# Performance work log

Measured on AMD Instinct MI355X. Metric: run time of the kernel, lower is better.

## Reference

```python
import jax, jax.numpy as jnp
import numpy as np

B, C, IMG, PS, S, D, H, HD, L, OUT = 512, 3, 36, 6, 36, 768, 12, 64, 4, 256

def _pos_embedding(seq_len, dim):
    # NOTE: cos at even indices, sin at odd (as in the torch source)
    position = np.arange(seq_len, dtype=np.float32)[:, None]
    div = np.exp(np.arange(0, dim, 2, dtype=np.float32) * -(np.log(10000.0) / dim))
    emb = np.zeros((seq_len, dim), dtype=np.float32)
    emb[:, 0::2] = np.cos(position * div)
    emb[:, 1::2] = np.sin(position * div)
    return jnp.asarray(emb)

def setup_inputs():
    ks = jax.random.split(jax.random.key(0), 10)
    sc = lambda f: 1.0 / np.sqrt(f)
    return {
        'batch': jax.random.normal(ks[0], (B, C, IMG, IMG), jnp.float32),
        'W_patch': jax.random.normal(ks[1], (D, PS * PS), jnp.float32) * sc(PS * PS),
        'b_patch': jnp.zeros((D,), jnp.float32),
        'pos': _pos_embedding(S, D),
        'ln1_g': jnp.ones((L, D), jnp.float32),
        'ln1_b': jnp.zeros((L, D), jnp.float32),
        'Wq': jax.random.normal(ks[2], (L, H, HD, HD), jnp.float32) * sc(HD),
        'bq': jnp.zeros((L, H, HD), jnp.float32),
        'Wk': jax.random.normal(ks[3], (L, H, HD, HD), jnp.float32) * sc(HD),
        'bk': jnp.zeros((L, H, HD), jnp.float32),
        'Wv': jax.random.normal(ks[4], (L, H, HD, HD), jnp.float32) * sc(HD),
        'bv': jnp.zeros((L, H, HD), jnp.float32),
        'ln2_g': jnp.ones((L, D), jnp.float32),
        'ln2_b': jnp.zeros((L, D), jnp.float32),
        'W1': jax.random.normal(ks[5], (L, 2 * D, D), jnp.float32) * sc(D),
        'b1': jnp.zeros((L, 2 * D), jnp.float32),
        'W2': jax.random.normal(ks[6], (L, D, 2 * D), jnp.float32) * sc(2 * D),
        'b2': jnp.zeros((L, D), jnp.float32),
        'W_out': jax.random.normal(ks[7], (OUT, D), jnp.float32) * sc(D),
        'b_out': jnp.zeros((OUT,), jnp.float32),
    }

def _layernorm(x, g, b):
    m = jnp.mean(x, axis=-1, keepdims=True)
    v = jnp.mean((x - m) ** 2, axis=-1, keepdims=True)
    return (x - m) / jnp.sqrt(v + 1e-5) * g + b

def _forward(batch, W_patch, b_patch, pos, ln1_g, ln1_b, Wq, bq, Wk, bk, Wv, bv,
             ln2_g, ln2_b, W1, b1, W2, b2, W_out, b_out):
    b_, c_ = batch.shape[0], batch.shape[1]
    # patchify: (B,C,36,36) -> (B,C,36 patches,36 pixels), matching torch unfold+reshape
    p = batch.reshape(b_, c_, IMG // PS, PS, IMG // PS, PS)
    p = p.transpose(0, 1, 2, 4, 3, 5).reshape(b_, c_, S, PS * PS)
    z = p @ W_patch.T + b_patch + pos  # pos broadcasts over (B,C)
    scale = 1.0 / np.sqrt(HD)
    for l in range(L):
        # pre-LN then batched per-head attention (collapses the python loops)
        h = _layernorm(z, ln1_g[l], ln1_b[l]).reshape(b_, c_, S, H, HD)
        q = jnp.einsum('bcshd,hed->bcshe', h, Wq[l]) + bq[l]
        k = jnp.einsum('bcshd,hed->bcshe', h, Wk[l]) + bk[l]
        v = jnp.einsum('bcshd,hed->bcshe', h, Wv[l]) + bv[l]
        attn = jax.nn.softmax(jnp.einsum('bcshe,bcthe->bchst', q, k) * scale, axis=-1)
        o = jnp.einsum('bchst,bcthe->bcshe', attn, v).reshape(b_, c_, S, D)
        z = z + o
        z = _layernorm(z, ln2_g[l], ln2_b[l])
        z = z + (jax.nn.relu(z @ W1[l].T + b1[l]) @ W2[l].T + b2[l])
    return z @ W_out.T + b_out

def reference(batch, W_patch, b_patch, pos, ln1_g, ln1_b, Wq, bq, Wk, bk, Wv, bv,
              ln2_g, ln2_b, W1, b1, W2, b2, W_out, b_out):
    return _forward(batch, W_patch, b_patch, pos, ln1_g, ln1_b, Wq, bq, Wk, bk, Wv, bv,
                    ln2_g, ln2_b, W1, b1, W2, b2, W_out, b_out)
```

## Files before the change

### kernel.cpp

```cpp
#include <hip/hip_runtime.h>
#include <hip/hip_bf16.h>
#include <cstdint>
#include <cstddef>

typedef __bf16 bf16;
typedef bf16 bf16x8 __attribute__((ext_vector_type(8)));
typedef bf16 bf16x4 __attribute__((ext_vector_type(4)));
typedef float f32x4 __attribute__((ext_vector_type(4)));
typedef unsigned int u32;

#define GLD_LDS16(gptr, lptr)                                                        \
  __builtin_amdgcn_global_load_lds((const __attribute__((address_space(1))) u32*)(gptr), \
                                   (__attribute__((address_space(3))) u32*)(lptr), 16, 0, 0)

static constexpr int S = 36, D = 768, H = 12, HD = 64, DFF = 1536;
static constexpr int BC = 1536;
static constexpr int M = BC * S;
static constexpr int OUTD = 256;

__global__ __launch_bounds__(256) void f2b_kernel(const float* __restrict__ in,
                                                  bf16* __restrict__ out, int n4) {
  int i = blockIdx.x * 256 + threadIdx.x;
  if (i < n4) {
    float4 f = ((const float4*)in)[i];
    bf16x4 o = {(bf16)f.x, (bf16)f.y, (bf16)f.z, (bf16)f.w};
    ((bf16x4*)out)[i] = o;
  }
}

__global__ __launch_bounds__(256) void patch_embed(const float* __restrict__ batch,
                                                   const float* __restrict__ Wp,
                                                   const float* __restrict__ bp,
                                                   const float* __restrict__ pos,
                                                   float* __restrict__ z) {
  int bc = blockIdx.x, tid = threadIdx.x;
  __shared__ float p[36][40];
  for (int i = tid; i < 1296; i += 256) {
    float f = batch[(size_t)bc * 1296 + i];
    int row = i / 36, col = i - row * 36;
    p[(row / 6) * 6 + col / 6][(row % 6) * 6 + (col % 6)] = f;
  }
  __syncthreads();
  for (int c0 = 0; c0 < 768; c0 += 256) {
    int d = c0 + tid;
    float wr[36];
    const float4* wp4 = (const float4*)(Wp + (size_t)d * 36);
#pragma unroll
    for (int q = 0; q < 9; ++q) {
      float4 f = wp4[q];
      wr[q * 4] = f.x; wr[q * 4 + 1] = f.y; wr[q * 4 + 2] = f.z; wr[q * 4 + 3] = f.w;
    }
    float gb = bp[d];
    for (int s = 0; s < 36; ++s) {
      float acc = 0.f;
#pragma unroll
      for (int k = 0; k < 36; ++k) acc += p[s][k] * wr[k];
      z[((size_t)bc * 36 + s) * 768 + d] = acc + gb + pos[s * 768 + d];
    }
  }
}

__global__ __launch_bounds__(256) void ln_stats(const float* __restrict__ zin,
                                                float* __restrict__ stats) {
  int row = blockIdx.x * 4 + (threadIdx.x >> 6);
  int lane = threadIdx.x & 63;
  const float* zr = zin + (size_t)row * D;
  float x[12];
#pragma unroll
  for (int i = 0; i < 12; ++i) x[i] = zr[i * 64 + lane];
  float s = 0.f;
#pragma unroll
  for (int i = 0; i < 12; ++i) s += x[i];
#pragma unroll
  for (int off = 32; off >= 1; off >>= 1) s += __shfl_xor(s, off, 64);
  float m = s * (1.f / 768.f);
  float v = 0.f;
#pragma unroll
  for (int i = 0; i < 12; ++i) { float dd = x[i] - m; v += dd * dd; }
#pragma unroll
  for (int off = 32; off >= 1; off >>= 1) v += __shfl_xor(v, off, 64);
  v *= (1.f / 768.f);
  if (lane == 0) {
    stats[(size_t)row * 2] = m;
    stats[(size_t)row * 2 + 1] = rsqrtf(v + 1e-5f);
  }
}

__global__ __launch_bounds__(256) void ln_inplace(float* __restrict__ z,
                                                  const float* __restrict__ g,
                                                  const float* __restrict__ bt) {
  int row = blockIdx.x * 4 + (threadIdx.x >> 6);
  int lane = threadIdx.x & 63;
  float* zr = z + (size_t)row * D;
  float x[12];
#pragma unroll
  for (int i = 0; i < 12; ++i) x[i] = zr[i * 64 + lane];
  float s = 0.f;
#pragma unroll
  for (int i = 0; i < 12; ++i) s += x[i];
#pragma unroll
  for (int off = 32; off >= 1; off >>= 1) s += __shfl_xor(s, off, 64);
  float m = s * (1.f / 768.f);
  float v = 0.f;
#pragma unroll
  for (int i = 0; i < 12; ++i) { float dd = x[i] - m; v += dd * dd; }
#pragma unroll
  for (int off = 32; off >= 1; off >>= 1) v += __shfl_xor(v, off, 64);
  v *= (1.f / 768.f);
  float rstd = rsqrtf(v + 1e-5f);
#pragma unroll
  for (int i = 0; i < 12; ++i) {
    int d = i * 64 + lane;
    zr[d] = (x[i] - m) * rstd * g[d] + bt[d];
  }
}

__global__ __launch_bounds__(64) void attn_kernel(const float* __restrict__ zg,
                                                  const float* __restrict__ stats,
                                                  const float* __restrict__ g1,
                                                  const float* __restrict__ b1_,
                                                  const bf16* __restrict__ Wq,
                                                  const bf16* __restrict__ Wk,
                                                  const bf16* __restrict__ Wv,
                                                  const float* __restrict__ bq,
                                                  const float* __restrict__ bk,
                                                  const float* __restrict__ bv,
                                                  float* __restrict__ z) {
  int head = blockIdx.x;
  int bc = blockIdx.y;
  __shared__ __align__(16) bf16 qb[48 * 72];
  __shared__ __align__(16) bf16 kb[48 * 72];
  __shared__ __align__(16) bf16 vt[64 * 72];
  int lane = threadIdx.x;
  int lr = lane & 15, quad = lane >> 4;

#pragma unroll
  for (int t0 = 0; t0 < 16; ++t0) vt[lane * 72 + 48 + t0] = (bf16)0.f;

  const float* zsrc = zg + ((size_t)bc * S) * D + head * HD;
  const float* st = stats + (size_t)bc * S * 2;

  float gv[2][8], bvv[2][8];
#pragma unroll
  for (int kt = 0; kt < 2; ++kt) {
    int c0 = head * HD + kt * 32 + quad * 8;
    float4 ga = *(const float4*)(g1 + c0);
    float4 gb2 = *(const float4*)(g1 + c0 + 4);
    float4 ba = *(const float4*)(b1_ + c0);
    float4 bb2 = *(const float4*)(b1_ + c0 + 4);
    gv[kt][0] = ga.x; gv[kt][1] = ga.y; gv[kt][2] = ga.z; gv[kt][3] = ga.w;
    gv[kt][4] = gb2.x; gv[kt][5] = gb2.y; gv[kt][6] = gb2.z; gv[kt][7] = gb2.w;
    bvv[kt][0] = ba.x; bvv[kt][1] = ba.y; bvv[kt][2] = ba.z; bvv[kt][3] = ba.w;
    bvv[kt][4] = bb2.x; bvv[kt][5] = bb2.y; bvv[kt][6] = bb2.z; bvv[kt][7] = bb2.w;
  }

  bf16x8 hfrag[3][2];
#pragma unroll
  for (int mt = 0; mt < 3; ++mt) {
    int srow = mt * 16 + lr;
    if (srow < 36) {
      float mm = st[srow * 2], rr = st[srow * 2 + 1];
#pragma unroll
      for (int kt = 0; kt < 2; ++kt) {
        int c0 = kt * 32 + quad * 8;
        float4 f0 = *(const float4*)(zsrc + (size_t)srow * D + c0);
        float4 f1 = *(const float4*)(zsrc + (size_t)srow * D + c0 + 4);
        float hv[8] = {f0.x, f0.y, f0.z, f0.w, f1.x, f1.y, f1.z, f1.w};
        bf16x8 o;
#pragma unroll
        for (int j = 0; j < 8; ++j) o[j] = (bf16)((hv[j] - mm) * rr * gv[kt][j] + bvv[kt][j]);
        hfrag[mt][kt] = o;
      }
    } else {
#pragma unroll
      for (int kt = 0; kt < 2; ++kt) {
        bf16x8 o;
#pragma unroll
        for (int j = 0; j < 8; ++j) o[j] = (bf16)0.f;
        hfrag[mt][kt] = o;
      }
    }
  }

  const bf16* Wm[3] = {Wq + (size_t)head * 4096, Wk + (size_t)head * 4096, Wv + (size_t)head * 4096};
  const float* Bm[3] = {bq + head * 64, bk + head * 64, bv + head * 64};
  for (int p = 0; p < 3; ++p) {
    bf16x8 bfr[4][2];
#pragma unroll
    for (int nt = 0; nt < 4; ++nt)
#pragma unroll
      for (int kt = 0; kt < 2; ++kt)
        bfr[nt][kt] = *(const bf16x8*)(Wm[p] + (nt * 16 + lr) * 64 + kt * 32 + quad * 8);
#pragma unroll
    for (int mt = 0; mt < 3; ++mt) {
      f32x4 acc[4] = {};
#pragma unroll
      for (int kt = 0; kt < 2; ++kt)
#pragma unroll
        for (int nt = 0; nt < 4; ++nt)
          acc[nt] = __builtin_amdgcn_mfma_f32_16x16x32_bf16(hfrag[mt][kt], bfr[nt][kt], acc[nt], 0, 0, 0);
#pragma unroll
      for (int nt = 0; nt < 4; ++nt) {
        float bb = Bm[p][nt * 16 + lr];
#pragma unroll
        for (int r = 0; r < 4; ++r) {
          int s2 = mt * 16 + quad * 4 + r;
          int e = nt * 16 + lr;
          float val = acc[nt][r] + bb;
          if (p == 0) qb[s2 * 72 + e] = (bf16)val;
          else if (p == 1) kb[s2 * 72 + e] = (bf16)val;
          else vt[e * 72 + s2] = (bf16)val;
        }
      }
    }
  }
  __syncthreads();

  f32x4 sc[3][3];
#pragma unroll
  for (int mt = 0; mt < 3; ++mt)
#pragma unroll
    for (int nt = 0; nt < 3; ++nt) {
      f32x4 a = {};
#pragma unroll
      for (int kt = 0; kt < 2; ++kt) {
        bf16x8 af = *(const bf16x8*)&qb[(mt * 16 + lr) * 72 + kt * 32 + quad * 8];
        bf16x8 bf_ = *(const bf16x8*)&kb[(nt * 16 + lr) * 72 + kt * 32 + quad * 8];
        a = __builtin_amdgcn_mfma_f32_16x16x32_bf16(af, bf_, a, 0, 0, 0);
      }
      int t = nt * 16 + lr;
#pragma unroll
      for (int r = 0; r < 4; ++r) {
        float v = a[r] * 0.125f;
        if (t >= 36) v = -1e30f;
        sc[mt][nt][r] = v;
      }
    }
  __syncthreads();

#pragma unroll
  for (int mt = 0; mt < 3; ++mt) {
    float mx[4], sum[4];
#pragma unroll
    for (int r = 0; r < 4; ++r)
      mx[r] = fmaxf(fmaxf(sc[mt][0][r], sc[mt][1][r]), sc[mt][2][r]);
#pragma unroll
    for (int r = 0; r < 4; ++r)
#pragma unroll
      for (int off = 8; off >= 1; off >>= 1) mx[r] = fmaxf(mx[r], __shfl_xor(mx[r], off, 64));
#pragma unroll
    for (int r = 0; r < 4; ++r) sum[r] = 0.f;
#pragma unroll
    for (int nt = 0; nt < 3; ++nt)
#pragma unroll
      for (int r = 0; r < 4; ++r) {
        float e = __expf(sc[mt][nt][r] - mx[r]);
        sc[mt][nt][r] = e;
        sum[r] += e;
      }
#pragma unroll
    for (int r = 0; r < 4; ++r)
#pragma unroll
      for (int off = 8; off >= 1; off >>= 1) sum[r] += __shfl_xor(sum[r], off, 64);
#pragma unroll
    for (int nt = 0; nt < 4; ++nt)
#pragma unroll
      for (int r = 0; r < 4; ++r) {
        int s2 = mt * 16 + quad * 4 + r;
        int t = nt * 16 + lr;
        float pv = (nt < 3) ? sc[mt][nt][r] / sum[r] : 0.f;
        qb[s2 * 72 + t] = (bf16)pv;
      }
  }
  __syncthreads();

#pragma unroll
  for (int mt = 0; mt < 3; ++mt) {
    f32x4 o[4] = {};
#pragma unroll
    for (int kt = 0; kt < 2; ++kt) {
      bf16x8 a = *(const bf16x8*)&qb[(mt * 16 + lr) * 72 + kt * 32 + quad * 8];
#pragma unroll
      for (int nt = 0; nt < 4; ++nt) {
        bf16x8 b = *(const bf16x8*)&vt[(nt * 16 + lr) * 72 + kt * 32 + quad * 8];
        o[nt] = __builtin_amdgcn_mfma_f32_16x16x32_bf16(a, b, o[nt], 0, 0, 0);
      }
    }
#pragma unroll
    for (int nt = 0; nt < 4; ++nt)
#pragma unroll
      for (int r = 0; r < 4; ++r) {
        int s2 = mt * 16 + quad * 4 + r;
        if (s2 < 36) {
          int e = nt * 16 + lr;
          size_t idx = ((size_t)bc * S + s2) * D + head * HD + e;
          z[idx] += o[nt][r];
        }
      }
  }
}

template <int N, int K, int MODE, int AF32>
__global__ __launch_bounds__(256) void gemm_bt(const void* __restrict__ A,
                                               const bf16* __restrict__ Bw,
                                               const float* __restrict__ bias,
                                               const float* __restrict__ res,
                                               void* __restrict__ outp) {
  constexpr int BK = 64;
  __shared__ __align__(16) bf16 As[128 * BK];
  __shared__ __align__(16) bf16 Bs[128 * BK];
  int tid = threadIdx.x;
  int bn = blockIdx.x, bm = blockIdx.y;
  const bf16* Abf = (const bf16*)A + (size_t)bm * 128 * K;
  const float* Af = (const float*)A + (size_t)bm * 128 * K;
  const bf16* Bb = Bw + (size_t)bn * 128 * K;
  int lane = tid & 63, wave = tid >> 6;
  int wm = (wave >> 1) * 64, wn = (wave & 1) * 64;
  int lr = lane & 15, quad = lane >> 4;
  f32x4 acc[4][4] = {};
  for (int k0 = 0; k0 < K; k0 += BK) {
    if (AF32) {
#pragma unroll
      for (int r = 0; r < 8; ++r) {
        int c = r * 256 + tid;
        int row = c >> 4, col4 = (c & 15) * 4;
        float4 f = *(const float4*)(Af + (size_t)row * K + k0 + col4);
        bf16x4 o = {(bf16)f.x, (bf16)f.y, (bf16)f.z, (bf16)f.w};
        *(bf16x4*)&As[row * BK + col4] = o;
      }
    } else {
#pragma unroll
      for (int r = 0; r < 4; ++r) {
        int c = r * 256 + tid;
        int row = c >> 3, col = (c & 7) * 8;
        GLD_LDS16(Abf + (size_t)row * K + k0 + col, &As[c * 8]);
      }
    }
#pragma unroll
    for (int r = 0; r < 4; ++r) {
      int c = r * 256 + tid;
      int row = c >> 3, col = (c & 7) * 8;
      GLD_LDS16(Bb + (size_t)row * K + k0 + col, &Bs[c * 8]);
    }
    __syncthreads();
#pragma unroll
    for (int kt = 0; kt < 2; ++kt) {
      bf16x8 af[4], bfr[4];
#pragma unroll
      for (int mt = 0; mt < 4; ++mt) af[mt] = *(const bf16x8*)&As[(wm + mt * 16 + lr) * BK + kt * 32 + quad * 8];
#pragma unroll
      for (int nt = 0; nt < 4; ++nt) bfr[nt] = *(const bf16x8*)&Bs[(wn + nt * 16 + lr) * BK + kt * 32 + quad * 8];
#pragma unroll
      for (int mt = 0; mt < 4; ++mt)
#pragma unroll
        for (int nt = 0; nt < 4; ++nt)
          acc[mt][nt] = __builtin_amdgcn_mfma_f32_16x16x32_bf16(af[mt], bfr[nt], acc[mt][nt], 0, 0, 0);
    }
    __syncthreads();
  }
  int row0 = bm * 128 + wm + quad * 4;
  int col0 = bn * 128 + wn + lr;
#pragma unroll
  for (int mt = 0; mt < 4; ++mt)
#pragma unroll
    for (int nt = 0; nt < 4; ++nt) {
      int col = col0 + nt * 16;
      float bv = bias[col];
#pragma unroll
      for (int r = 0; r < 4; ++r) {
        size_t idx = (size_t)(row0 + mt * 16 + r) * N + col;
        float v = acc[mt][nt][r] + bv;
        if (MODE == 0) ((bf16*)outp)[idx] = (bf16)fmaxf(v, 0.f);
        else if (MODE == 1) ((float*)outp)[idx] = v + res[idx];
        else ((float*)outp)[idx] = v;
      }
    }
}

extern "C" void kernel_launch(void* const* d_in, const int* in_sizes, int n_in,
                              void* d_out, int out_size, void* d_ws, size_t ws_size,
                              hipStream_t stream) {
  const float* batch   = (const float*)d_in[0];
  const float* W_patch = (const float*)d_in[1];
  const float* b_patch = (const float*)d_in[2];
  const float* pos     = (const float*)d_in[3];
  const float* ln1_g   = (const float*)d_in[4];
  const float* ln1_b   = (const float*)d_in[5];
  const float* Wq      = (const float*)d_in[6];
  const float* bq      = (const float*)d_in[7];
  const float* Wk      = (const float*)d_in[8];
  const float* bk      = (const float*)d_in[9];
  const float* Wv      = (const float*)d_in[10];
  const float* bv      = (const float*)d_in[11];
  const float* ln2_g   = (const float*)d_in[12];
  const float* ln2_b   = (const float*)d_in[13];
  const float* W1      = (const float*)d_in[14];
  const float* b1      = (const float*)d_in[15];
  const float* W2      = (const float*)d_in[16];
  const float* b2      = (const float*)d_in[17];
  const float* W_out   = (const float*)d_in[18];
  const float* b_out   = (const float*)d_in[19];
  float* out = (float*)d_out;

  char* ws = (char*)d_ws;
  size_t off = 0;
  float* z     = (float*)(ws + off); off += (size_t)M * D * 4;
  float* stats = (float*)(ws + off); off += (size_t)M * 2 * 4;
  bf16* wq_b = (bf16*)(ws + off);    off += (size_t)4 * H * 4096 * 2;
  bf16* wk_b = (bf16*)(ws + off);    off += (size_t)4 * H * 4096 * 2;
  bf16* wv_b = (bf16*)(ws + off);    off += (size_t)4 * H * 4096 * 2;
  bf16* w1_b = (bf16*)(ws + off);    off += (size_t)4 * DFF * D * 2;
  bf16* w2_b = (bf16*)(ws + off);    off += (size_t)4 * D * DFF * 2;
  bf16* wo_b = (bf16*)(ws + off);    off += (size_t)OUTD * D * 2;
  bf16* act  = (bf16*)(ws + off);

  size_t avail = ws_size > off ? ws_size - off : (size_t)0;
  long long rcl = (long long)(avail / ((size_t)DFF * 2));
  int rc = (rcl > (long long)M) ? M : (int)rcl;
  rc = (rc / 128) * 128;
  if (rc <= 0) rc = 128;

  f2b_kernel<<<192, 256, 0, stream>>>(Wq, wq_b, 49152);
  f2b_kernel<<<192, 256, 0, stream>>>(Wk, wk_b, 49152);
  f2b_kernel<<<192, 256, 0, stream>>>(Wv, wv_b, 49152);
  f2b_kernel<<<4608, 256, 0, stream>>>(W1, w1_b, 1179648);
  f2b_kernel<<<4608, 256, 0, stream>>>(W2, w2_b, 1179648);
  f2b_kernel<<<192, 256, 0, stream>>>(W_out, wo_b, 49152);

  patch_embed<<<BC, 256, 0, stream>>>(batch, W_patch, b_patch, pos, z);

  for (int l = 0; l < 4; ++l) {
    ln_stats<<<M / 4, 256, 0, stream>>>(z, stats);
    attn_kernel<<<dim3(H, BC), 64, 0, stream>>>(z, stats, ln1_g + l * D, ln1_b + l * D,
        wq_b + (size_t)l * H * 4096, wk_b + (size_t)l * H * 4096, wv_b + (size_t)l * H * 4096,
        bq + l * H * 64, bk + l * H * 64, bv + l * H * 64, z);
    ln_inplace<<<M / 4, 256, 0, stream>>>(z, ln2_g + l * D, ln2_b + l * D);
    for (int m0 = 0; m0 < M; m0 += rc) {
      int mr = (M - m0 < rc) ? (M - m0) : rc;
      gemm_bt<DFF, D, 0, 1><<<dim3(DFF / 128, mr / 128), 256, 0, stream>>>(
          z + (size_t)m0 * D, w1_b + (size_t)l * DFF * D, b1 + l * DFF, nullptr, act);
      gemm_bt<D, DFF, 1, 0><<<dim3(D / 128, mr / 128), 256, 0, stream>>>(
          act, w2_b + (size_t)l * D * DFF, b2 + l * D, z + (size_t)m0 * D, z + (size_t)m0 * D);
    }
  }

  gemm_bt<OUTD, D, 2, 1><<<dim3(OUTD / 128, M / 128), 256, 0, stream>>>(
      z, wo_b, b_out, nullptr, out);
}
```

Measured before the change: 3.510 ms.

## Split attention kernel across three waves for Q/K/V and row tiles

```diff
diff --git a/kernel.cpp b/kernel.cpp
--- a/kernel.cpp
+++ b/kernel.cpp
@@ -115,27 +115,31 @@
   }
 }
 
-__global__ __launch_bounds__(64) void attn_kernel(const float* __restrict__ zg,
-                                                  const float* __restrict__ stats,
-                                                  const float* __restrict__ g1,
-                                                  const float* __restrict__ b1_,
-                                                  const bf16* __restrict__ Wq,
-                                                  const bf16* __restrict__ Wk,
-                                                  const bf16* __restrict__ Wv,
-                                                  const float* __restrict__ bq,
-                                                  const float* __restrict__ bk,
-                                                  const float* __restrict__ bv,
-                                                  float* __restrict__ z) {
+__global__ __launch_bounds__(192) void attn_kernel(const float* __restrict__ zg,
+                                                   const float* __restrict__ stats,
+                                                   const float* __restrict__ g1,
+                                                   const float* __restrict__ b1_,
+                                                   const bf16* __restrict__ Wq,
+                                                   const bf16* __restrict__ Wk,
+                                                   const bf16* __restrict__ Wv,
+                                                   const float* __restrict__ bq,
+                                                   const float* __restrict__ bk,
+                                                   const float* __restrict__ bv,
+                                                   float* __restrict__ z) {
   int head = blockIdx.x;
   int bc = blockIdx.y;
   __shared__ __align__(16) bf16 qb[48 * 72];
   __shared__ __align__(16) bf16 kb[48 * 72];
   __shared__ __align__(16) bf16 vt[64 * 72];
-  int lane = threadIdx.x;
+  int tid = threadIdx.x;
+  int wave = tid >> 6;
+  int lane = tid & 63;
   int lr = lane & 15, quad = lane >> 4;
 
-#pragma unroll
-  for (int t0 = 0; t0 < 16; ++t0) vt[lane * 72 + 48 + t0] = (bf16)0.f;
+  if (wave == 2) {
+#pragma unroll
+    for (int t0 = 0; t0 < 16; ++t0) vt[lane * 72 + 48 + t0] = (bf16)0.f;
+  }
 
   const float* zsrc = zg + ((size_t)bc * S) * D + head * HD;
   const float* st = stats + (size_t)bc * S * 2;
@@ -182,15 +186,15 @@
     }
   }
 
-  const bf16* Wm[3] = {Wq + (size_t)head * 4096, Wk + (size_t)head * 4096, Wv + (size_t)head * 4096};
-  const float* Bm[3] = {bq + head * 64, bk + head * 64, bv + head * 64};
-  for (int p = 0; p < 3; ++p) {
+  {
+    const bf16* Wm = (wave == 0 ? Wq : wave == 1 ? Wk : Wv) + (size_t)head * 4096;
+    const float* Bm = (wave == 0 ? bq : wave == 1 ? bk : bv) + head * 64;
     bf16x8 bfr[4][2];
 #pragma unroll
     for (int nt = 0; nt < 4; ++nt)
 #pragma unroll
       for (int kt = 0; kt < 2; ++kt)
-        bfr[nt][kt] = *(const bf16x8*)(Wm[p] + (nt * 16 + lr) * 64 + kt * 32 + quad * 8);
+        bfr[nt][kt] = *(const bf16x8*)(Wm + (nt * 16 + lr) * 64 + kt * 32 + quad * 8);
 #pragma unroll
     for (int mt = 0; mt < 3; ++mt) {
       f32x4 acc[4] = {};
@@ -201,14 +205,14 @@
           acc[nt] = __builtin_amdgcn_mfma_f32_16x16x32_bf16(hfrag[mt][kt], bfr[nt][kt], acc[nt], 0, 0, 0);
 #pragma unroll
       for (int nt = 0; nt < 4; ++nt) {
-        float bb = Bm[p][nt * 16 + lr];
+        float bb = Bm[nt * 16 + lr];
 #pragma unroll
         for (int r = 0; r < 4; ++r) {
           int s2 = mt * 16 + quad * 4 + r;
           int e = nt * 16 + lr;
           float val = acc[nt][r] + bb;
-          if (p == 0) qb[s2 * 72 + e] = (bf16)val;
-          else if (p == 1) kb[s2 * 72 + e] = (bf16)val;
+          if (wave == 0) qb[s2 * 72 + e] = (bf16)val;
+          else if (wave == 1) kb[s2 * 72 + e] = (bf16)val;
           else vt[e * 72 + s2] = (bf16)val;
         }
       }
@@ -216,46 +220,44 @@
   }
   __syncthreads();
 
-  f32x4 sc[3][3];
-#pragma unroll
-  for (int mt = 0; mt < 3; ++mt)
-#pragma unroll
-    for (int nt = 0; nt < 3; ++nt) {
-      f32x4 a = {};
-#pragma unroll
-      for (int kt = 0; kt < 2; ++kt) {
-        bf16x8 af = *(const bf16x8*)&qb[(mt * 16 + lr) * 72 + kt * 32 + quad * 8];
-        bf16x8 bf_ = *(const bf16x8*)&kb[(nt * 16 + lr) * 72 + kt * 32 + quad * 8];
-        a = __builtin_amdgcn_mfma_f32_16x16x32_bf16(af, bf_, a, 0, 0, 0);
-      }
-      int t = nt * 16 + lr;
+  int mt = wave;
+
+  f32x4 sc[3];
+#pragma unroll
+  for (int nt = 0; nt < 3; ++nt) {
+    f32x4 a = {};
+#pragma unroll
+    for (int kt = 0; kt < 2; ++kt) {
+      bf16x8 af = *(const bf16x8*)&qb[(mt * 16 + lr) * 72 + kt * 32 + quad * 8];
+      bf16x8 bf_ = *(const bf16x8*)&kb[(nt * 16 + lr) * 72 + kt * 32 + quad * 8];
+      a = __builtin_amdgcn_mfma_f32_16x16x32_bf16(af, bf_, a, 0, 0, 0);
+    }
+    int t = nt * 16 + lr;
+#pragma unroll
+    for (int r = 0; r < 4; ++r) {
+      float v = a[r] * 0.125f;
+      if (t >= 36) v = -1e30f;
+      sc[nt][r] = v;
+    }
+  }
+
+  {
+    float mx[4], sum[4];
+#pragma unroll
+    for (int r = 0; r < 4; ++r)
+      mx[r] = fmaxf(fmaxf(sc[0][r], sc[1][r]), sc[2][r]);
+#pragma unroll
+    for (int r = 0; r < 4; ++r)
+#pragma unroll
+      for (int off = 8; off >= 1; off >>= 1) mx[r] = fmaxf(mx[r], __shfl_xor(mx[r], off, 64));
+#pragma unroll
+    for (int r = 0; r < 4; ++r) sum[r] = 0.f;
+#pragma unroll
+    for (int nt = 0; nt < 3; ++nt)
 #pragma unroll
       for (int r = 0; r < 4; ++r) {
-        float v = a[r] * 0.125f;
-        if (t >= 36) v = -1e30f;
-        sc[mt][nt][r] = v;
-      }
-    }
-  __syncthreads();
-
-#pragma unroll
-  for (int mt = 0; mt < 3; ++mt) {
-    float mx[4], sum[4];
-#pragma unroll
-    for (int r = 0; r < 4; ++r)
-      mx[r] = fmaxf(fmaxf(sc[mt][0][r], sc[mt][1][r]), sc[mt][2][r]);
-#pragma unroll
-    for (int r = 0; r < 4; ++r)
-#pragma unroll
-      for (int off = 8; off >= 1; off >>= 1) mx[r] = fmaxf(mx[r], __shfl_xor(mx[r], off, 64));
-#pragma unroll
-    for (int r = 0; r < 4; ++r) sum[r] = 0.f;
-#pragma unroll
-    for (int nt = 0; nt < 3; ++nt)
-#pragma unroll
-      for (int r = 0; r < 4; ++r) {
-        float e = __expf(sc[mt][nt][r] - mx[r]);
-        sc[mt][nt][r] = e;
+        float e = __expf(sc[nt][r] - mx[r]);
+        sc[nt][r] = e;
         sum[r] += e;
       }
 #pragma unroll
@@ -268,14 +270,12 @@
       for (int r = 0; r < 4; ++r) {
         int s2 = mt * 16 + quad * 4 + r;
         int t = nt * 16 + lr;
-        float pv = (nt < 3) ? sc[mt][nt][r] / sum[r] : 0.f;
+        float pv = (nt < 3) ? sc[nt][r] / sum[r] : 0.f;
         qb[s2 * 72 + t] = (bf16)pv;
       }
   }
-  __syncthreads();
-
-#pragma unroll
-  for (int mt = 0; mt < 3; ++mt) {
+
+  {
     f32x4 o[4] = {};
 #pragma unroll
     for (int kt = 0; kt < 2; ++kt) {
@@ -431,7 +431,7 @@
 
   for (int l = 0; l < 4; ++l) {
     ln_stats<<<M / 4, 256, 0, stream>>>(z, stats);
-    attn_kernel<<<dim3(H, BC), 64, 0, stream>>>(z, stats, ln1_g + l * D, ln1_b + l * D,
+    attn_kernel<<<dim3(H, BC), 192, 0, stream>>>(z, stats, ln1_g + l * D, ln1_b + l * D,
         wq_b + (size_t)l * H * 4096, wk_b + (size_t)l * H * 4096, wv_b + (size_t)l * H * 4096,
         bq + l * H * 64, bk + l * H * 64, bv + l * H * 64, z);
     ln_inplace<<<M / 4, 256, 0, stream>>>(z, ln2_g + l * D, ln2_b + l * D);
```

Result: slower. 3.726 ms (+6.2%).

## Fold Wq and Wk into one per-head bilinear matrix for attention scores

Applied to the files above, without the earlier changes.

```diff
diff --git a/kernel.cpp b/kernel.cpp
--- a/kernel.cpp
+++ b/kernel.cpp
@@ -26,6 +26,43 @@
     bf16x4 o = {(bf16)f.x, (bf16)f.y, (bf16)f.z, (bf16)f.w};
     ((bf16x4*)out)[i] = o;
   }
+}
+
+__global__ __launch_bounds__(64) void qk_prep(const float* __restrict__ Wq,
+                                              const float* __restrict__ Wk,
+                                              const float* __restrict__ bq,
+                                              bf16* __restrict__ wb,
+                                              float* __restrict__ vkout) {
+  int lh = blockIdx.x;
+  int e = threadIdx.x;
+  __shared__ float Wqs[64][64];
+  __shared__ float Wks[64][64];
+  const float* wqp = Wq + (size_t)lh * 4096;
+  const float* wkp = Wk + (size_t)lh * 4096;
+  for (int i = e; i < 4096; i += 64) {
+    Wqs[i >> 6][i & 63] = wqp[i];
+    Wks[i >> 6][i & 63] = wkp[i];
+  }
+  __syncthreads();
+  float ks[64];
+#pragma unroll
+  for (int f = 0; f < 64; ++f) ks[f] = Wks[f][e];
+  for (int d0 = 0; d0 < 64; d0 += 4) {
+    float a0 = 0.f, a1 = 0.f, a2 = 0.f, a3 = 0.f;
+#pragma unroll
+    for (int f = 0; f < 64; ++f) {
+      float4 wq4 = *(const float4*)&Wqs[f][d0];
+      a0 += wq4.x * ks[f]; a1 += wq4.y * ks[f];
+      a2 += wq4.z * ks[f]; a3 += wq4.w * ks[f];
+    }
+    bf16x4 o = {(bf16)a0, (bf16)a1, (bf16)a2, (bf16)a3};
+    *(bf16x4*)&wb[(size_t)lh * 4096 + e * 64 + d0] = o;
+  }
+  const float* bqp = bq + lh * 64;
+  float acc = 0.f;
+#pragma unroll
+  for (int f = 0; f < 64; ++f) acc += ks[f] * bqp[f];
+  vkout[lh * 64 + e] = acc;
 }
 
 __global__ __launch_bounds__(256) void patch_embed(const float* __restrict__ batch,
@@ -119,17 +156,14 @@
                                                   const float* __restrict__ stats,
                                                   const float* __restrict__ g1,
                                                   const float* __restrict__ b1_,
-                                                  const bf16* __restrict__ Wq,
-                                                  const bf16* __restrict__ Wk,
+                                                  const bf16* __restrict__ Wqk,
                                                   const bf16* __restrict__ Wv,
-                                                  const float* __restrict__ bq,
-                                                  const float* __restrict__ bk,
+                                                  const float* __restrict__ vk,
                                                   const float* __restrict__ bv,
                                                   float* __restrict__ z) {
   int head = blockIdx.x;
   int bc = blockIdx.y;
-  __shared__ __align__(16) bf16 qb[48 * 72];
-  __shared__ __align__(16) bf16 kb[48 * 72];
+  __shared__ __align__(16) bf16 gb[48 * 72];
   __shared__ __align__(16) bf16 vt[64 * 72];
   int lane = threadIdx.x;
   int lr = lane & 15, quad = lane >> 4;
@@ -182,9 +216,31 @@
     }
   }
 
-  const bf16* Wm[3] = {Wq + (size_t)head * 4096, Wk + (size_t)head * 4096, Wv + (size_t)head * 4096};
-  const float* Bm[3] = {bq + head * 64, bk + head * 64, bv + head * 64};
-  for (int p = 0; p < 3; ++p) {
+  float vkv[2][8];
+#pragma unroll
+  for (int kt = 0; kt < 2; ++kt) {
+    int c0 = head * 64 + kt * 32 + quad * 8;
+    float4 va = *(const float4*)(vk + c0);
+    float4 vb2 = *(const float4*)(vk + c0 + 4);
+    vkv[kt][0] = va.x; vkv[kt][1] = va.y; vkv[kt][2] = va.z; vkv[kt][3] = va.w;
+    vkv[kt][4] = vb2.x; vkv[kt][5] = vb2.y; vkv[kt][6] = vb2.z; vkv[kt][7] = vb2.w;
+  }
+  float tv[3];
+#pragma unroll
+  for (int mt = 0; mt < 3; ++mt) {
+    float sp = 0.f;
+#pragma unroll
+    for (int kt = 0; kt < 2; ++kt)
+#pragma unroll
+      for (int j = 0; j < 8; ++j) sp += (float)hfrag[mt][kt][j] * vkv[kt][j];
+    sp += __shfl_xor(sp, 16, 64);
+    sp += __shfl_xor(sp, 32, 64);
+    tv[mt] = sp;
+  }
+
+  const bf16* Wm[2] = {Wqk + (size_t)head * 4096, Wv + (size_t)head * 4096};
+  const float* bvp = bv + head * 64;
+  for (int p = 0; p < 2; ++p) {
     bf16x8 bfr[4][2];
 #pragma unroll
     for (int nt = 0; nt < 4; ++nt)
@@ -201,14 +257,13 @@
           acc[nt] = __builtin_amdgcn_mfma_f32_16x16x32_bf16(hfrag[mt][kt], bfr[nt][kt], acc[nt], 0, 0, 0);
 #pragma unroll
       for (int nt = 0; nt < 4; ++nt) {
-        float bb = Bm[p][nt * 16 + lr];
+        float bb = (p == 1) ? bvp[nt * 16 + lr] : 0.f;
 #pragma unroll
         for (int r = 0; r < 4; ++r) {
           int s2 = mt * 16 + quad * 4 + r;
           int e = nt * 16 + lr;
           float val = acc[nt][r] + bb;
-          if (p == 0) qb[s2 * 72 + e] = (bf16)val;
-          else if (p == 1) kb[s2 * 72 + e] = (bf16)val;
+          if (p == 0) gb[s2 * 72 + e] = (bf16)val;
           else vt[e * 72 + s2] = (bf16)val;
         }
       }
@@ -224,14 +279,13 @@
       f32x4 a = {};
 #pragma unroll
       for (int kt = 0; kt < 2; ++kt) {
-        bf16x8 af = *(const bf16x8*)&qb[(mt * 16 + lr) * 72 + kt * 32 + quad * 8];
-        bf16x8 bf_ = *(const bf16x8*)&kb[(nt * 16 + lr) * 72 + kt * 32 + quad * 8];
-        a = __builtin_amdgcn_mfma_f32_16x16x32_bf16(af, bf_, a, 0, 0, 0);
+        bf16x8 af = *(const bf16x8*)&gb[(mt * 16 + lr) * 72 + kt * 32 + quad * 8];
+        a = __builtin_amdgcn_mfma_f32_16x16x32_bf16(af, hfrag[nt][kt], a, 0, 0, 0);
       }
       int t = nt * 16 + lr;
 #pragma unroll
       for (int r = 0; r < 4; ++r) {
-        float v = a[r] * 0.125f;
+        float v = (a[r] + tv[nt]) * 0.125f;
         if (t >= 36) v = -1e30f;
         sc[mt][nt][r] = v;
       }
@@ -269,7 +323,7 @@
         int s2 = mt * 16 + quad * 4 + r;
         int t = nt * 16 + lr;
         float pv = (nt < 3) ? sc[mt][nt][r] / sum[r] : 0.f;
-        qb[s2 * 72 + t] = (bf16)pv;
+        gb[s2 * 72 + t] = (bf16)pv;
       }
   }
   __syncthreads();
@@ -279,7 +333,7 @@
     f32x4 o[4] = {};
 #pragma unroll
     for (int kt = 0; kt < 2; ++kt) {
-      bf16x8 a = *(const bf16x8*)&qb[(mt * 16 + lr) * 72 + kt * 32 + quad * 8];
+      bf16x8 a = *(const bf16x8*)&gb[(mt * 16 + lr) * 72 + kt * 32 + quad * 8];
 #pragma unroll
       for (int nt = 0; nt < 4; ++nt) {
         bf16x8 b = *(const bf16x8*)&vt[(nt * 16 + lr) * 72 + kt * 32 + quad * 8];
@@ -401,14 +455,15 @@
   const float* W_out   = (const float*)d_in[18];
   const float* b_out   = (const float*)d_in[19];
   float* out = (float*)d_out;
+  (void)bk;
 
   char* ws = (char*)d_ws;
   size_t off = 0;
   float* z     = (float*)(ws + off); off += (size_t)M * D * 4;
   float* stats = (float*)(ws + off); off += (size_t)M * 2 * 4;
-  bf16* wq_b = (bf16*)(ws + off);    off += (size_t)4 * H * 4096 * 2;
-  bf16* wk_b = (bf16*)(ws + off);    off += (size_t)4 * H * 4096 * 2;
+  bf16* wqk_b = (bf16*)(ws + off);   off += (size_t)4 * H * 4096 * 2;
   bf16* wv_b = (bf16*)(ws + off);    off += (size_t)4 * H * 4096 * 2;
+  float* vk_f = (float*)(ws + off);  off += (size_t)4 * H * 64 * 4;
   bf16* w1_b = (bf16*)(ws + off);    off += (size_t)4 * DFF * D * 2;
   bf16* w2_b = (bf16*)(ws + off);    off += (size_t)4 * D * DFF * 2;
   bf16* wo_b = (bf16*)(ws + off);    off += (size_t)OUTD * D * 2;
@@ -420,8 +475,7 @@
   rc = (rc / 128) * 128;
   if (rc <= 0) rc = 128;
 
-  f2b_kernel<<<192, 256, 0, stream>>>(Wq, wq_b, 49152);
-  f2b_kernel<<<192, 256, 0, stream>>>(Wk, wk_b, 49152);
+  qk_prep<<<48, 64, 0, stream>>>(Wq, Wk, bq, wqk_b, vk_f);
   f2b_kernel<<<192, 256, 0, stream>>>(Wv, wv_b, 49152);
   f2b_kernel<<<4608, 256, 0, stream>>>(W1, w1_b, 1179648);
   f2b_kernel<<<4608, 256, 0, stream>>>(W2, w2_b, 1179648);
@@ -432,8 +486,8 @@
   for (int l = 0; l < 4; ++l) {
     ln_stats<<<M / 4, 256, 0, stream>>>(z, stats);
     attn_kernel<<<dim3(H, BC), 64, 0, stream>>>(z, stats, ln1_g + l * D, ln1_b + l * D,
-        wq_b + (size_t)l * H * 4096, wk_b + (size_t)l * H * 4096, wv_b + (size_t)l * H * 4096,
-        bq + l * H * 64, bk + l * H * 64, bv + l * H * 64, z);
+        wqk_b + (size_t)l * H * 4096, wv_b + (size_t)l * H * 4096,
+        vk_f + (size_t)l * H * 64, bv + (size_t)l * H * 64, z);
     ln_inplace<<<M / 4, 256, 0, stream>>>(z, ln2_g + l * D, ln2_b + l * D);
     for (int m0 = 0; m0 < M; m0 += rc) {
       int mr = (M - m0 < rc) ? (M - m0) : rc;
```

Result: faster. 3.440 ms (-2.0%).
